# Kernel optimization log

Hardware: AMD Instinct MI355X
Metric: run time of the kernel (lower is better)

The kernel has to match this reference:

```python
import jax, jax.numpy as jnp
import numpy as np

N = 50000      # nodes
E = 800000     # edges
F_IN = 9       # node features
H = 128        # model_units
G = 64         # graphs in batch


def _lin_init(key, fan_in, fan_out):
    k1, k2 = jax.random.split(key)
    lim = 1.0 / np.sqrt(fan_in)
    W = jax.random.uniform(k1, (fan_in, fan_out), minval=-lim, maxval=lim, dtype=jnp.float32)
    b = jax.random.uniform(k2, (fan_out,), minval=-lim, maxval=lim, dtype=jnp.float32)
    return W, b


def setup_inputs() -> dict:
    key = jax.random.key(0)
    ks = jax.random.split(key, 12)
    x = jax.random.normal(ks[0], (N, F_IN), dtype=jnp.float32)
    edge_index = jax.random.randint(ks[1], (2, E), 0, N, dtype=jnp.int32)
    batch = jnp.sort(jax.random.randint(ks[2], (N,), 0, G, dtype=jnp.int32))
    W1, b1 = _lin_init(ks[3], F_IN, H)      # conv1 (GCN)
    W2, b2 = _lin_init(ks[4], H, H)         # conv2 (GCN, shared across layers)
    We1, be1 = _lin_init(ks[5], 2 * H, H)   # EdgeConv MLP layer 1
    We2, be2 = _lin_init(ks[6], H, H)       # EdgeConv MLP layer 2
    Wf1, bf1 = _lin_init(ks[7], H, H)
    Wf2, bf2 = _lin_init(ks[8], H, 32)
    Wf3, bf3 = _lin_init(ks[9], 32, 1)
    return {"x": x, "edge_index": edge_index, "batch": batch,
            "W1": W1, "b1": b1, "W2": W2, "b2": b2,
            "We1": We1, "be1": be1, "We2": We2, "be2": be2,
            "Wf1": Wf1, "bf1": bf1, "Wf2": Wf2, "bf2": bf2,
            "Wf3": Wf3, "bf3": bf3}


def _gcn(x, W, b, src, dst, dis):
    # GCNConv with implicit self-loops and symmetric normalization.
    h = x @ W                                              # [N,H]
    msg = h[src] * dis[src, None]                          # gather + scale
    agg = jax.ops.segment_sum(msg, dst, num_segments=N)    # scatter-add
    return dis[:, None] * agg + h * (dis * dis)[:, None] + b


def _edgeconv(x, We1, be1, We2, be2, src, dst):
    # EdgeConv: max_j MLP([x_i, x_j - x_i]) over incoming edges j->i.
    xi = x[dst]                                            # [E,H]
    xj = x[src]
    m = jnp.concatenate([xi, xj - xi], axis=-1)            # [E,2H]
    m = jax.nn.relu(m @ We1 + be1) @ We2 + be2             # [E,H]
    agg = jax.ops.segment_max(m, dst, num_segments=N)
    return jnp.where(jnp.isfinite(agg), agg, 0.0)          # isolated nodes -> 0


def reference(x, edge_index, batch, W1, b1, W2, b2, We1, be1, We2, be2,
              Wf1, bf1, Wf2, bf2, Wf3, bf3):
    src, dst = edge_index[0], edge_index[1]
    # degree (with self loop) for GCN normalization
    deg = jax.ops.segment_sum(jnp.ones((E,), jnp.float32), dst, num_segments=N) + 1.0
    dis = jax.lax.rsqrt(deg)

    h = jnp.tanh(_gcn(x, W1, b1, src, dst, dis))
    h = jnp.tanh(_edgeconv(h, We1, be1, We2, be2, src, dst))
    # model_layers = 3 -> loop body once, then final block (dropout = identity, eval)
    for _ in range(2):
        h = jnp.tanh(_gcn(h, W2, b2, src, dst, dis))
        h = jnp.tanh(_edgeconv(h, We1, be1, We2, be2, src, dst))

    h = jnp.tanh(h @ Wf1 + bf1)
    h = jnp.tanh(h @ Wf2 + bf2)
    h = h @ Wf3 + bf3                                      # [N,1]

    counts = jax.ops.segment_sum(jnp.ones((N,), jnp.float32), batch, num_segments=G)
    pooled = jax.ops.segment_sum(h, batch, num_segments=G) / jnp.maximum(counts, 1.0)[:, None]
    return jax.nn.sigmoid(pooled)                          # [G,1]
```

## Files before the change

kernel.cpp:

```cpp
#include <hip/hip_runtime.h>
#include <hip/hip_bf16.h>

#define N_NODES 50000
#define N_EDGES 800000
#define F_IN 9
#define H 128
#define G_GRAPHS 64
#define HH (H * H)
#define MAXT (N_EDGES / 16 + N_NODES)

typedef short bf16x8 __attribute__((ext_vector_type(8)));
typedef float f32x4 __attribute__((ext_vector_type(4)));

static __device__ inline short f2b(float f) {
    __hip_bfloat16 h = __float2bfloat16(f);
    return *reinterpret_cast<short*>(&h);
}
static __device__ inline float blo(unsigned u) { return __uint_as_float(u << 16); }
static __device__ inline float bhi(unsigned u) { return __uint_as_float(u & 0xFFFF0000u); }
static __device__ inline unsigned encodef(float f) {
    unsigned u = __float_as_uint(f);
    return (u & 0x80000000u) ? ~u : (u | 0x80000000u);
}
static __device__ inline float decodef(unsigned u) {
    return __uint_as_float((u & 0x80000000u) ? (u ^ 0x80000000u) : ~u);
}

__global__ __launch_bounds__(256) void k_detect(const unsigned* __restrict__ x, int* flag) {
    __shared__ int cnt;
    if (threadIdx.x == 0) cnt = 0;
    __syncthreads();
    unsigned u = x[threadIdx.x];
    int e = (u >> 7) & 0xFF;
    if (e >= 0x70 && e <= 0x83) atomicAdd(&cnt, 1);
    __syncthreads();
    if (threadIdx.x == 0) *flag = (cnt >= 128) ? 1 : 0;
}

struct CvtArgs { const void* src[15]; float* dst[15]; };

__global__ __launch_bounds__(256) void k_cvt_all(CvtArgs a, const int* __restrict__ flag) {
    const int sz[15] = {450000, 1152, 128, 16384, 128, 32768, 128, 16384, 128,
                        16384, 128, 4096, 32, 32, 1};
    int i = blockIdx.x * 256 + threadIdx.x;
    int fl = *flag;
    int base = 0;
    #pragma unroll
    for (int s = 0; s < 15; ++s) {
        if (i >= base && i < base + sz[s]) {
            int off = i - base;
            float v = fl ? __bfloat162float(((const __hip_bfloat16*)a.src[s])[off])
                         : ((const float*)a.src[s])[off];
            a.dst[s][off] = v;
        }
        base += sz[s];
    }
}

__global__ __launch_bounds__(256) void k_zero(float* p, int n) {
    int i = blockIdx.x * 256 + threadIdx.x;
    if (i < n) p[i] = 0.f;
}

__global__ __launch_bounds__(256) void k_sub(float* w) {
    int i = blockIdx.x * 256 + threadIdx.x;
    if (i < HH) w[i] -= w[HH + i];
}

__global__ __launch_bounds__(256) void k_prep(const float* __restrict__ W,
                                              short* __restrict__ Wf, int NT) {
    int tid = blockIdx.x * 256 + threadIdx.x;
    int total = 4 * NT * 64;
    if (tid >= total) return;
    int kc = tid / (NT * 64);
    int ct = (tid / 64) % NT;
    int lane = tid & 63;
    int Nc = NT * 16;
    int kb = kc * 32 + (lane >> 4) * 8;
    int col = ct * 16 + (lane & 15);
    #pragma unroll
    for (int j = 0; j < 8; ++j)
        Wf[tid * 8 + j] = f2b(W[(kb + j) * Nc + col]);
}

__global__ __launch_bounds__(256) void k_hist(const int* __restrict__ dst, int* cnt) {
    int e = blockIdx.x * 256 + threadIdx.x;
    if (e < N_EDGES) atomicAdd(&cnt[dst[e]], 1);
}

__global__ __launch_bounds__(256) void k_scan1(const int* __restrict__ deg, int* __restrict__ out,
                                               int* __restrict__ blockSums) {
    __shared__ int lds[256];
    int base = blockIdx.x * 2048;
    int t = threadIdx.x;
    int local[8];
    int s = 0;
    #pragma unroll
    for (int j = 0; j < 8; ++j) {
        int idx = base + t * 8 + j;
        int v = (idx < N_NODES) ? deg[idx] : 0;
        local[j] = s;
        s += v;
    }
    lds[t] = s;
    __syncthreads();
    if (t == 0) {
        int run = 0;
        for (int i = 0; i < 256; ++i) { int v = lds[i]; lds[i] = run; run += v; }
        blockSums[blockIdx.x] = run;
    }
    __syncthreads();
    int offs = lds[t];
    #pragma unroll
    for (int j = 0; j < 8; ++j) {
        int idx = base + t * 8 + j;
        if (idx < N_NODES) out[idx] = offs + local[j];
    }
}

__global__ void k_scan2(int* blockSums, int nb, int* rowptr) {
    int run = 0;
    for (int i = 0; i < nb; ++i) { int v = blockSums[i]; blockSums[i] = run; run += v; }
    rowptr[N_NODES] = N_EDGES;
}

__global__ void k_scan2t(int* blockSums, int nb, int* tstart, int* ntiles) {
    int run = 0;
    for (int i = 0; i < nb; ++i) { int v = blockSums[i]; blockSums[i] = run; run += v; }
    tstart[N_NODES] = run;
    *ntiles = run;
}

__global__ __launch_bounds__(256) void k_scan3(int* rowptr, const int* __restrict__ blockSums) {
    int idx = blockIdx.x * 256 + threadIdx.x;
    if (idx < N_NODES) rowptr[idx] += blockSums[idx >> 11];
}

__global__ __launch_bounds__(256) void k_scatter(const int* __restrict__ src, const int* __restrict__ dst,
                                                 const int* __restrict__ rowptr, int* cursor,
                                                 int* __restrict__ csr_src) {
    int e = blockIdx.x * 256 + threadIdx.x;
    if (e >= N_EDGES) return;
    int d = dst[e];
    int pos = rowptr[d] + atomicAdd(&cursor[d], 1);
    csr_src[pos] = src[e];
}

__global__ __launch_bounds__(256) void k_dis_tcnt(const int* __restrict__ rowptr, float* dis, int* tcnt) {
    int n = blockIdx.x * 256 + threadIdx.x;
    if (n < N_NODES) {
        int deg = rowptr[n + 1] - rowptr[n];
        dis[n] = rsqrtf((float)deg + 1.0f);
        tcnt[n] = (deg + 15) >> 4;
    }
}

__global__ __launch_bounds__(256) void k_tfill(const int* __restrict__ rowptr,
                                               const int* __restrict__ csr_src,
                                               const int* __restrict__ tstart,
                                               int* __restrict__ tileN,
                                               int* __restrict__ tileSrc) {
    int n = blockIdx.x * 256 + threadIdx.x;
    if (n >= N_NODES) return;
    int t0 = tstart[n], t1 = tstart[n + 1];
    int beg = rowptr[n], end = rowptr[n + 1];
    for (int t = t0; t < t1; ++t) {
        tileN[t] = n;
        int tb = beg + (t - t0) * 16;
        #pragma unroll 4
        for (int j = 0; j < 16; ++j) {
            int ei = tb + j;
            tileSrc[t * 16 + j] = csr_src[ei < end ? ei : end - 1];
        }
    }
}

__global__ __launch_bounds__(256) void k_counts(const int* __restrict__ batch, float* counts) {
    __shared__ float lc[G_GRAPHS];
    int tid = threadIdx.x;
    if (tid < G_GRAPHS) lc[tid] = 0.f;
    __syncthreads();
    int n = blockIdx.x * 256 + tid;
    if (n < N_NODES) atomicAdd(&lc[batch[n]], 1.0f);
    __syncthreads();
    if (tid < G_GRAPHS && lc[tid] > 0.f) atomicAdd(&counts[tid], lc[tid]);
}

__global__ __launch_bounds__(256) void k_gemm_f32bf_scale(const float* __restrict__ A,
                                                          const float* __restrict__ W,
                                                          const float* __restrict__ dis,
                                                          short* __restrict__ out, int M) {
    __shared__ float w_lds[F_IN * H];
    for (int i = threadIdx.x; i < F_IN * H; i += 256) w_lds[i] = W[i];
    __syncthreads();
    int row = blockIdx.x * 8 + threadIdx.x / 32;
    int c4 = (threadIdx.x & 31) << 2;
    if (row >= M) return;
    const float* a = A + (size_t)row * F_IN;
    float acc0 = 0.f, acc1 = 0.f, acc2 = 0.f, acc3 = 0.f;
    #pragma unroll
    for (int k = 0; k < F_IN; ++k) {
        float av = a[k];
        float4 w = *reinterpret_cast<const float4*>(&w_lds[k * H + c4]);
        acc0 = fmaf(av, w.x, acc0);
        acc1 = fmaf(av, w.y, acc1);
        acc2 = fmaf(av, w.z, acc2);
        acc3 = fmaf(av, w.w, acc3);
    }
    float dv = dis[row];
    short* op = &out[(size_t)row * H + c4];
    op[0] = f2b(acc0 * dv); op[1] = f2b(acc1 * dv);
    op[2] = f2b(acc2 * dv); op[3] = f2b(acc3 * dv);
}

__global__ __launch_bounds__(512) void k_gemm_dual(const short* __restrict__ A,
                                                   const short* __restrict__ WfU,
                                                   const short* __restrict__ WfV,
                                                   const float* __restrict__ be1,
                                                   short* __restrict__ U,
                                                   short* __restrict__ V, int M) {
    __shared__ short wl[32768];
    for (int i = threadIdx.x * 8; i < 16384; i += 4096) {
        *reinterpret_cast<f32x4*>(&wl[i])         = *reinterpret_cast<const f32x4*>(&WfU[i]);
        *reinterpret_cast<f32x4*>(&wl[16384 + i]) = *reinterpret_cast<const f32x4*>(&WfV[i]);
    }
    __syncthreads();
    int wv = threadIdx.x >> 6, lane = threadIdx.x & 63;
    int er = lane & 15, kg = lane >> 4;
    int row0 = (blockIdx.x * 8 + wv) * 16;
    if (row0 >= M) return;
    bf16x8 af[4];
    #pragma unroll
    for (int kc = 0; kc < 4; ++kc)
        af[kc] = *reinterpret_cast<const bf16x8*>(&A[(size_t)(row0 + er) * H + kc * 32 + kg * 8]);
    const f32x4 vzero = {0.f, 0.f, 0.f, 0.f};
    f32x4 acc[8];
    #pragma unroll
    for (int ct = 0; ct < 8; ++ct) acc[ct] = vzero;
    #pragma unroll
    for (int kc = 0; kc < 4; ++kc)
        #pragma unroll
        for (int ct = 0; ct < 8; ++ct) {
            bf16x8 bf = *reinterpret_cast<const bf16x8*>(&wl[((kc * 8 + ct) * 64 + lane) * 8]);
            acc[ct] = __builtin_amdgcn_mfma_f32_16x16x32_bf16(af[kc], bf, acc[ct], 0, 0, 0);
        }
    #pragma unroll
    for (int ct = 0; ct < 8; ++ct) {
        int col = ct * 16 + er;
        float bv = be1[col];
        #pragma unroll
        for (int r = 0; r < 4; ++r)
            U[(size_t)(row0 + kg * 4 + r) * H + col] = f2b(acc[ct][r] + bv);
    }
    #pragma unroll
    for (int ct = 0; ct < 8; ++ct) acc[ct] = vzero;
    #pragma unroll
    for (int kc = 0; kc < 4; ++kc)
        #pragma unroll
        for (int ct = 0; ct < 8; ++ct) {
            bf16x8 bf = *reinterpret_cast<const bf16x8*>(&wl[16384 + ((kc * 8 + ct) * 64 + lane) * 8]);
            acc[ct] = __builtin_amdgcn_mfma_f32_16x16x32_bf16(af[kc], bf, acc[ct], 0, 0, 0);
        }
    #pragma unroll
    for (int ct = 0; ct < 8; ++ct) {
        int col = ct * 16 + er;
        #pragma unroll
        for (int r = 0; r < 4; ++r)
            V[(size_t)(row0 + kg * 4 + r) * H + col] = f2b(acc[ct][r]);
    }
}

__global__ __launch_bounds__(512) void k_gemm_scale(const short* __restrict__ A,
                                                    const short* __restrict__ Wf,
                                                    const float* __restrict__ dis,
                                                    short* __restrict__ out, int M) {
    __shared__ short wl[16384];
    for (int i = threadIdx.x * 8; i < 16384; i += 4096)
        *reinterpret_cast<f32x4*>(&wl[i]) = *reinterpret_cast<const f32x4*>(&Wf[i]);
    __syncthreads();
    int wv = threadIdx.x >> 6, lane = threadIdx.x & 63;
    int er = lane & 15, kg = lane >> 4;
    int row0 = (blockIdx.x * 8 + wv) * 16;
    if (row0 >= M) return;
    bf16x8 af[4];
    #pragma unroll
    for (int kc = 0; kc < 4; ++kc)
        af[kc] = *reinterpret_cast<const bf16x8*>(&A[(size_t)(row0 + er) * H + kc * 32 + kg * 8]);
    const f32x4 vzero = {0.f, 0.f, 0.f, 0.f};
    f32x4 acc[8];
    #pragma unroll
    for (int ct = 0; ct < 8; ++ct) acc[ct] = vzero;
    #pragma unroll
    for (int kc = 0; kc < 4; ++kc)
        #pragma unroll
        for (int ct = 0; ct < 8; ++ct) {
            bf16x8 bf = *reinterpret_cast<const bf16x8*>(&wl[((kc * 8 + ct) * 64 + lane) * 8]);
            acc[ct] = __builtin_amdgcn_mfma_f32_16x16x32_bf16(af[kc], bf, acc[ct], 0, 0, 0);
        }
    float dv[4];
    #pragma unroll
    for (int r = 0; r < 4; ++r) dv[r] = dis[row0 + kg * 4 + r];
    #pragma unroll
    for (int ct = 0; ct < 8; ++ct) {
        int col = ct * 16 + er;
        #pragma unroll
        for (int r = 0; r < 4; ++r)
            out[(size_t)(row0 + kg * 4 + r) * H + col] = f2b(acc[ct][r] * dv[r]);
    }
}

__global__ __launch_bounds__(256) void k_gcn_fused(const int* __restrict__ rowptr,
                                                   const int* __restrict__ csr_src,
                                                   const short* __restrict__ hWs,
                                                   const float* __restrict__ dis,
                                                   const float* __restrict__ bias,
                                                   short* __restrict__ out) {
    int wv = threadIdx.x >> 6, lane = threadIdx.x & 63;
    const unsigned* hw = (const unsigned*)hWs;
    for (int n = blockIdx.x * 4 + wv; n < N_NODES; n += gridDim.x * 4) {
        int beg = rowptr[n], end = rowptr[n + 1];
        float a0 = 0.f, a1 = 0.f, b0 = 0.f, b1 = 0.f;
        float c0 = 0.f, c1 = 0.f, d0 = 0.f, d1 = 0.f;
        int e = beg;
        for (; e + 8 <= end; e += 8) {
            int s0 = csr_src[e],     s1 = csr_src[e + 1], s2 = csr_src[e + 2], s3 = csr_src[e + 3];
            int s4 = csr_src[e + 4], s5 = csr_src[e + 5], s6 = csr_src[e + 6], s7 = csr_src[e + 7];
            unsigned w0 = hw[(size_t)s0 * 64 + lane];
            unsigned w1 = hw[(size_t)s1 * 64 + lane];
            unsigned w2 = hw[(size_t)s2 * 64 + lane];
            unsigned w3 = hw[(size_t)s3 * 64 + lane];
            unsigned w4 = hw[(size_t)s4 * 64 + lane];
            unsigned w5 = hw[(size_t)s5 * 64 + lane];
            unsigned w6 = hw[(size_t)s6 * 64 + lane];
            unsigned w7 = hw[(size_t)s7 * 64 + lane];
            a0 += blo(w0); a1 += bhi(w0);
            b0 += blo(w1); b1 += bhi(w1);
            c0 += blo(w2); c1 += bhi(w2);
            d0 += blo(w3); d1 += bhi(w3);
            a0 += blo(w4); a1 += bhi(w4);
            b0 += blo(w5); b1 += bhi(w5);
            c0 += blo(w6); c1 += bhi(w6);
            d0 += blo(w7); d1 += bhi(w7);
        }
        for (; e + 4 <= end; e += 4) {
            int s0 = csr_src[e], s1 = csr_src[e + 1], s2 = csr_src[e + 2], s3 = csr_src[e + 3];
            unsigned w0 = hw[(size_t)s0 * 64 + lane];
            unsigned w1 = hw[(size_t)s1 * 64 + lane];
            unsigned w2 = hw[(size_t)s2 * 64 + lane];
            unsigned w3 = hw[(size_t)s3 * 64 + lane];
            a0 += blo(w0); a1 += bhi(w0);
            b0 += blo(w1); b1 += bhi(w1);
            c0 += blo(w2); c1 += bhi(w2);
            d0 += blo(w3); d1 += bhi(w3);
        }
        for (; e < end; ++e) {
            unsigned w = hw[(size_t)csr_src[e] * 64 + lane];
            a0 += blo(w); a1 += bhi(w);
        }
        float s0f = (a0 + b0) + (c0 + d0);
        float s1f = (a1 + b1) + (c1 + d1);
        float dn = dis[n];
        unsigned wn = hw[(size_t)n * 64 + lane];
        float r0 = tanhf(dn * (s0f + blo(wn)) + bias[lane * 2]);
        float r1 = tanhf(dn * (s1f + bhi(wn)) + bias[lane * 2 + 1]);
        unsigned o = (unsigned)(unsigned short)f2b(r0) | ((unsigned)(unsigned short)f2b(r1) << 16);
        *reinterpret_cast<unsigned*>(&out[(size_t)n * H + lane * 2]) = o;
    }
}

__global__ __launch_bounds__(512) void k_edge_tile(const int* __restrict__ tileN,
                                                   const int* __restrict__ tileSrc,
                                                   const int* __restrict__ ntilesp,
                                                   const short* __restrict__ U,
                                                   const short* __restrict__ V,
                                                   const short* __restrict__ We2f,
                                                   unsigned* aggEnc) {
    int nt = *ntilesp;
    if ((int)(blockIdx.x * 8) >= nt) return;
    __shared__ short wl[16384];
    for (int i = threadIdx.x * 8; i < 16384; i += 4096)
        *reinterpret_cast<f32x4*>(&wl[i]) = *reinterpret_cast<const f32x4*>(&We2f[i]);
    __syncthreads();
    int wv = threadIdx.x >> 6, lane = threadIdx.x & 63;
    int er = lane & 15, kg = lane >> 4, kseg = kg * 8;
    int tid = blockIdx.x * 8 + wv;
    if (tid >= nt) return;
    int n = tileN[tid];
    int s = tileSrc[tid * 16 + er];
    const f32x4 vzero = {0.f, 0.f, 0.f, 0.f};
    f32x4 acc[8];
    #pragma unroll
    for (int ct = 0; ct < 8; ++ct) acc[ct] = vzero;
    #pragma unroll
    for (int kc = 0; kc < 4; ++kc) {
        uint4 uu4 = *reinterpret_cast<const uint4*>(&U[(size_t)n * H + kc * 32 + kseg]);
        uint4 vv4 = *reinterpret_cast<const uint4*>(&V[(size_t)s * H + kc * 32 + kseg]);
        bf16x8 af;
        unsigned uu, vv;
        uu = uu4.x; vv = vv4.x;
        af[0] = f2b(fmaxf(blo(uu) + blo(vv), 0.f));
        af[1] = f2b(fmaxf(bhi(uu) + bhi(vv), 0.f));
        uu = uu4.y; vv = vv4.y;
        af[2] = f2b(fmaxf(blo(uu) + blo(vv), 0.f));
        af[3] = f2b(fmaxf(bhi(uu) + bhi(vv), 0.f));
        uu = uu4.z; vv = vv4.z;
        af[4] = f2b(fmaxf(blo(uu) + blo(vv), 0.f));
        af[5] = f2b(fmaxf(bhi(uu) + bhi(vv), 0.f));
        uu = uu4.w; vv = vv4.w;
        af[6] = f2b(fmaxf(blo(uu) + blo(vv), 0.f));
        af[7] = f2b(fmaxf(bhi(uu) + bhi(vv), 0.f));
        #pragma unroll
        for (int ct = 0; ct < 8; ++ct) {
            bf16x8 bf = *reinterpret_cast<const bf16x8*>(&wl[((kc * 8 + ct) * 64 + lane) * 8]);
            acc[ct] = __builtin_amdgcn_mfma_f32_16x16x32_bf16(af, bf, acc[ct], 0, 0, 0);
        }
    }
    float cm[8];
    #pragma unroll
    for (int ct = 0; ct < 8; ++ct) {
        float v = fmaxf(fmaxf(acc[ct][0], acc[ct][1]), fmaxf(acc[ct][2], acc[ct][3]));
        v = fmaxf(v, __shfl_xor(v, 16));
        v = fmaxf(v, __shfl_xor(v, 32));
        cm[ct] = v;
    }
    float vA, vB;
    if (kg == 0)      { vA = cm[0]; vB = cm[1]; }
    else if (kg == 1) { vA = cm[2]; vB = cm[3]; }
    else if (kg == 2) { vA = cm[4]; vB = cm[5]; }
    else              { vA = cm[6]; vB = cm[7]; }
    int colA = (kg * 2) * 16 + er;
    int colB = (kg * 2 + 1) * 16 + er;
    atomicMax(&aggEnc[(size_t)n * H + colA], encodef(vA));
    atomicMax(&aggEnc[(size_t)n * H + colB], encodef(vB));
}

__global__ __launch_bounds__(256) void k_edge_combine(const unsigned* __restrict__ aggEnc,
                                                      const float* __restrict__ be2,
                                                      short* __restrict__ out) {
    int i = blockIdx.x * 256 + threadIdx.x;
    if (i >= N_NODES * 64) return;
    int n = i >> 6, c2 = (i & 63) << 1;
    unsigned u0 = aggEnc[(size_t)n * H + c2];
    unsigned u1 = aggEnc[(size_t)n * H + c2 + 1];
    float r0 = tanhf(u0 ? (decodef(u0) + be2[c2]) : 0.f);
    float r1 = tanhf(u1 ? (decodef(u1) + be2[c2 + 1]) : 0.f);
    unsigned o = (unsigned)(unsigned short)f2b(r0) | ((unsigned)(unsigned short)f2b(r1) << 16);
    *reinterpret_cast<unsigned*>(&out[(size_t)n * H + c2]) = o;
}

__global__ __launch_bounds__(512) void k_final_mlp(const short* __restrict__ h,
                                                   const short* __restrict__ WfF1,
                                                   const short* __restrict__ WfF2,
                                                   const float* __restrict__ bf1,
                                                   const float* __restrict__ bf2,
                                                   const float* __restrict__ Wf3,
                                                   const float* __restrict__ bf3,
                                                   const int* __restrict__ batch,
                                                   float* pooled, int M) {
    __shared__ short wl1[16384];
    __shared__ short wl2[4096];
    __shared__ short tb[8][2048];
    __shared__ float lp[G_GRAPHS];
    for (int i = threadIdx.x * 8; i < 16384; i += 4096)
        *reinterpret_cast<f32x4*>(&wl1[i]) = *reinterpret_cast<const f32x4*>(&WfF1[i]);
    if (threadIdx.x < 512) {
        int i = threadIdx.x * 8;
        if (i < 4096)
            *reinterpret_cast<f32x4*>(&wl2[i]) = *reinterpret_cast<const f32x4*>(&WfF2[i]);
    }
    if (threadIdx.x < G_GRAPHS) lp[threadIdx.x] = 0.f;
    __syncthreads();
    int wv = threadIdx.x >> 6, lane = threadIdx.x & 63;
    int er = lane & 15, kg = lane >> 4;
    int row0 = (blockIdx.x * 8 + wv) * 16;
    bool active = row0 < M;
    const f32x4 vzero = {0.f, 0.f, 0.f, 0.f};
    if (active) {
        bf16x8 af[4];
        #pragma unroll
        for (int kc = 0; kc < 4; ++kc)
            af[kc] = *reinterpret_cast<const bf16x8*>(&h[(size_t)(row0 + er) * H + kc * 32 + kg * 8]);
        f32x4 acc[8];
        #pragma unroll
        for (int ct = 0; ct < 8; ++ct) acc[ct] = vzero;
        #pragma unroll
        for (int kc = 0; kc < 4; ++kc)
            #pragma unroll
            for (int ct = 0; ct < 8; ++ct) {
                bf16x8 bf = *reinterpret_cast<const bf16x8*>(&wl1[((kc * 8 + ct) * 64 + lane) * 8]);
                acc[ct] = __builtin_amdgcn_mfma_f32_16x16x32_bf16(af[kc], bf, acc[ct], 0, 0, 0);
            }
        #pragma unroll
        for (int ct = 0; ct < 8; ++ct) {
            int col = ct * 16 + er;
            float bv = bf1[col];
            #pragma unroll
            for (int r = 0; r < 4; ++r)
                tb[wv][(kg * 4 + r) * 128 + col] = f2b(tanhf(acc[ct][r] + bv));
        }
    }
    __syncthreads();
    if (active) {
        bf16x8 af2[4];
        #pragma unroll
        for (int kc = 0; kc < 4; ++kc)
            af2[kc] = *reinterpret_cast<const bf16x8*>(&tb[wv][er * 128 + kc * 32 + kg * 8]);
        f32x4 a2[2];
        a2[0] = vzero; a2[1] = vzero;
        #pragma unroll
        for (int kc = 0; kc < 4; ++kc)
            #pragma unroll
            for (int ct = 0; ct < 2; ++ct) {
                bf16x8 bf = *reinterpret_cast<const bf16x8*>(&wl2[((kc * 2 + ct) * 64 + lane) * 8]);
                a2[ct] = __builtin_amdgcn_mfma_f32_16x16x32_bf16(af2[kc], bf, a2[ct], 0, 0, 0);
            }
        float w3a = Wf3[er], w3b = Wf3[16 + er];
        float b2a = bf2[er], b2b = bf2[16 + er];
        float bf3v = bf3[0];
        float psum[4];
        #pragma unroll
        for (int r = 0; r < 4; ++r) {
            float f2a = tanhf(a2[0][r] + b2a);
            float f2c = tanhf(a2[1][r] + b2b);
            float p = f2a * w3a + f2c * w3b;
            p += __shfl_xor(p, 1);
            p += __shfl_xor(p, 2);
            p += __shfl_xor(p, 4);
            p += __shfl_xor(p, 8);
            psum[r] = p + bf3v;
        }
        if (er == 0) {
            #pragma unroll
            for (int r = 0; r < 4; ++r) {
                int n = row0 + kg * 4 + r;
                if (n < M) atomicAdd(&lp[batch[n]], psum[r]);
            }
        }
    }
    __syncthreads();
    if (threadIdx.x < G_GRAPHS && lp[threadIdx.x] != 0.f)
        atomicAdd(&pooled[threadIdx.x], lp[threadIdx.x]);
}

__global__ __launch_bounds__(64) void k_final(const float* pooled, const float* counts,
                                              void* out, const int* __restrict__ flag) {
    int g = threadIdx.x;
    if (g < G_GRAPHS) {
        float v = pooled[g] / fmaxf(counts[g], 1.0f);
        float s = 1.0f / (1.0f + expf(-v));
        if (*flag) ((__hip_bfloat16*)out)[g] = __float2bfloat16(s);
        else       ((float*)out)[g] = s;
    }
}

extern "C" void kernel_launch(void* const* d_in, const int* in_sizes, int n_in,
                              void* d_out, int out_size, void* d_ws, size_t ws_size,
                              hipStream_t stream) {
    const int* ei    = (const int*)d_in[1];
    const int* src   = ei;
    const int* dst   = ei + N_EDGES;
    const int* batch = (const int*)d_in[2];

    float* ws = (float*)d_ws;
    size_t off = 0;
    auto alloc = [&](size_t n) { off = (off + 3) & ~(size_t)3; float* p = ws + off; off += n; return p; };

    const size_t NH = (size_t)N_NODES * H;
    short* hb     = (short*)alloc(NH / 2);
    short* Ub     = (short*)alloc(NH / 2);
    short* Vb     = (short*)alloc(NH / 2);
    unsigned* aggEnc = (unsigned*)alloc(NH);
    float* xf     = alloc((size_t)N_NODES * F_IN);
    float* dis    = alloc(N_NODES);
    float* pooled = alloc(G_GRAPHS);
    float* counts = alloc(G_GRAPHS);
    int*   flag   = (int*)alloc(1);
    int*   rowptr = (int*)alloc(N_NODES + 1);
    int*   cursor = (int*)alloc(N_NODES);
    int*   csrsrc = (int*)alloc(N_EDGES);
    int*   bsums  = (int*)alloc(32);
    int*   bsums2 = (int*)alloc(32);
    int*   tstart = (int*)alloc(N_NODES + 1);
    int*   ntiles = (int*)alloc(1);
    int*   tileN  = (int*)alloc(MAXT);
    int*   tileSrc= (int*)alloc((size_t)MAXT * 16);

    float* W1  = alloc(F_IN * H);
    float* b1  = alloc(H);
    float* W2  = alloc(HH);
    float* b2  = alloc(H);
    float* We1 = alloc(2 * HH);
    float* be1 = alloc(H);
    float* We2 = alloc(HH);
    float* be2 = alloc(H);
    float* Wf1 = alloc(HH);
    float* bf1 = alloc(H);
    float* Wf2 = alloc(H * 32);
    float* bf2 = alloc(32);
    float* Wf3 = alloc(32);
    float* bf3 = alloc(4);
    short* WfU  = (short*)alloc(8192);
    short* WfV  = (short*)alloc(8192);
    short* WfW2 = (short*)alloc(8192);
    short* WfF1 = (short*)alloc(8192);
    short* WfF2 = (short*)alloc(2048);
    short* We2f = (short*)alloc(8192);

    const int eB    = (N_EDGES + 255) / 256;
    const int nB    = (N_NODES + 255) / 256;
    const int scanB = (N_NODES + 2047) / 2048;
    const int mfmaB = (N_NODES / 16 + 7) / 8;
    const int gcnB  = (N_NODES + 3) / 4;
    const int tileB = (MAXT + 7) / 8;
    const int zAggB = (int)((NH + 255) / 256);
    const int combB = (N_NODES * 64 + 255) / 256;

    k_detect<<<1, 256, 0, stream>>>((const unsigned*)d_in[0], flag);

    CvtArgs ca;
    const int srcIdx[15] = {0, 3, 4, 5, 6, 7, 8, 9, 10, 11, 12, 13, 14, 15, 16};
    float* dsts[15] = {xf, W1, b1, W2, b2, We1, be1, We2, be2, Wf1, bf1, Wf2, bf2, Wf3, bf3};
    for (int s = 0; s < 15; ++s) { ca.src[s] = d_in[srcIdx[s]]; ca.dst[s] = dsts[s]; }
    const int cvtTotal = 450000 + 1152 + 128 + 16384 + 128 + 32768 + 128 + 16384 + 128
                       + 16384 + 128 + 4096 + 32 + 32 + 1;
    k_cvt_all<<<(cvtTotal + 255) / 256, 256, 0, stream>>>(ca, flag);

    k_sub<<<(HH + 255) / 256, 256, 0, stream>>>(We1);
    k_prep<<<8, 256, 0, stream>>>(We1, WfU, 8);
    k_prep<<<8, 256, 0, stream>>>(We1 + HH, WfV, 8);
    k_prep<<<8, 256, 0, stream>>>(W2, WfW2, 8);
    k_prep<<<8, 256, 0, stream>>>(Wf1, WfF1, 8);
    k_prep<<<2, 256, 0, stream>>>(Wf2, WfF2, 2);
    k_prep<<<8, 256, 0, stream>>>(We2, We2f, 8);

    k_zero<<<nB, 256, 0, stream>>>((float*)cursor, N_NODES);
    k_hist<<<eB, 256, 0, stream>>>(dst, cursor);
    k_scan1<<<scanB, 256, 0, stream>>>(cursor, rowptr, bsums);
    k_scan2<<<1, 1, 0, stream>>>(bsums, scanB, rowptr);
    k_scan3<<<nB, 256, 0, stream>>>(rowptr, bsums);
    k_zero<<<nB, 256, 0, stream>>>((float*)cursor, N_NODES);
    k_scatter<<<eB, 256, 0, stream>>>(src, dst, rowptr, cursor, csrsrc);
    k_dis_tcnt<<<nB, 256, 0, stream>>>(rowptr, dis, cursor);
    k_zero<<<1, 256, 0, stream>>>(pooled, 2 * G_GRAPHS);
    k_counts<<<nB, 256, 0, stream>>>(batch, counts);

    k_scan1<<<scanB, 256, 0, stream>>>(cursor, tstart, bsums2);
    k_scan2t<<<1, 1, 0, stream>>>(bsums2, scanB, tstart, ntiles);
    k_scan3<<<nB, 256, 0, stream>>>(tstart, bsums2);
    k_tfill<<<nB, 256, 0, stream>>>(rowptr, csrsrc, tstart, tileN, tileSrc);

    k_gemm_f32bf_scale<<<(N_NODES + 7) / 8, 256, 0, stream>>>(xf, W1, dis, Ub, N_NODES);
    k_gcn_fused<<<gcnB, 256, 0, stream>>>(rowptr, csrsrc, Ub, dis, b1, hb);

    for (int iter = 0; iter < 3; ++iter) {
        k_gemm_dual<<<mfmaB, 512, 0, stream>>>(hb, WfU, WfV, be1, Ub, Vb, N_NODES);
        k_zero<<<zAggB, 256, 0, stream>>>((float*)aggEnc, (int)NH);
        k_edge_tile<<<tileB, 512, 0, stream>>>(tileN, tileSrc, ntiles, Ub, Vb, We2f, aggEnc);
        k_edge_combine<<<combB, 256, 0, stream>>>(aggEnc, be2, hb);
        if (iter < 2) {
            k_gemm_scale<<<mfmaB, 512, 0, stream>>>(hb, WfW2, dis, Ub, N_NODES);
            k_gcn_fused<<<gcnB, 256, 0, stream>>>(rowptr, csrsrc, Ub, dis, b2, hb);
        }
    }

    k_final_mlp<<<mfmaB, 512, 0, stream>>>(hb, WfF1, WfF2, bf1, bf2, Wf3, bf3,
                                           batch, pooled, N_NODES);
    k_final<<<1, 64, 0, stream>>>(pooled, counts, d_out, flag);
}
```

Baseline: 559.2 us.

## Fuse edge-combine into downstream GEMMs and merge setup kernels and scans

Removes the separate edge-combine kernel. The next GEMM (GCN scale, or the final MLP) now reads the max-encoded aggregate directly, decodes it, adds the bias, applies tanh and packs to bf16 in registers. This saves a full N×H write and re-read of the intermediate bf16 features each layer. It also merges the weight-prep kernels, the two prefix scans and the counts/zeroing into fewer launches, and uses the packed bf16 convert instruction. The trade-off is redundant decode and tanh work in each GEMM block, plus reading 4-byte aggregates instead of 2-byte features.

```diff
diff --git a/kernel.cpp b/kernel.cpp
--- a/kernel.cpp
+++ b/kernel.cpp
@@ -25,14 +25,21 @@
 static __device__ inline float decodef(unsigned u) {
     return __uint_as_float((u & 0x80000000u) ? (u ^ 0x80000000u) : ~u);
 }
-
-__global__ __launch_bounds__(256) void k_detect(const unsigned* __restrict__ x, int* flag) {
+static __device__ inline unsigned cvtpk(float lo, float hi) {
+    unsigned r;
+    asm("v_cvt_pk_bf16_f32 %0, %1, %2" : "=v"(r) : "v"(lo), "v"(hi));
+    return r;
+}
+
+__global__ __launch_bounds__(256) void k_detect(const unsigned* __restrict__ x, int* flag,
+                                                float* pooled, float* counts) {
     __shared__ int cnt;
     if (threadIdx.x == 0) cnt = 0;
     __syncthreads();
     unsigned u = x[threadIdx.x];
     int e = (u >> 7) & 0xFF;
     if (e >= 0x70 && e <= 0x83) atomicAdd(&cnt, 1);
+    if (threadIdx.x < G_GRAPHS) { pooled[threadIdx.x] = 0.f; counts[threadIdx.x] = 0.f; }
     __syncthreads();
     if (threadIdx.x == 0) *flag = (cnt >= 128) ? 1 : 0;
 }
@@ -62,14 +69,21 @@
     if (i < n) p[i] = 0.f;
 }
 
-__global__ __launch_bounds__(256) void k_sub(float* w) {
-    int i = blockIdx.x * 256 + threadIdx.x;
-    if (i < HH) w[i] -= w[HH + i];
-}
-
-__global__ __launch_bounds__(256) void k_prep(const float* __restrict__ W,
-                                              short* __restrict__ Wf, int NT) {
-    int tid = blockIdx.x * 256 + threadIdx.x;
+__global__ __launch_bounds__(256) void k_prep_all(const float* __restrict__ We1,
+                                                  const float* __restrict__ W2,
+                                                  const float* __restrict__ Wf1,
+                                                  const float* __restrict__ Wf2,
+                                                  const float* __restrict__ We2,
+                                                  short* WfU, short* WfV, short* WfW2,
+                                                  short* WfF1, short* WfF2, short* We2f) {
+    int b = blockIdx.x;
+    const float* W; const float* Wm = nullptr; short* out; int NT = 8; int tid;
+    if (b < 8)       { W = We1;      Wm = We1 + HH; out = WfU;  tid = b * 256 + threadIdx.x; }
+    else if (b < 16) { W = We1 + HH; out = WfV;  tid = (b - 8) * 256 + threadIdx.x; }
+    else if (b < 24) { W = W2;       out = WfW2; tid = (b - 16) * 256 + threadIdx.x; }
+    else if (b < 32) { W = Wf1;      out = WfF1; tid = (b - 24) * 256 + threadIdx.x; }
+    else if (b < 40) { W = We2;      out = We2f; tid = (b - 32) * 256 + threadIdx.x; }
+    else             { W = Wf2;      out = WfF2; NT = 2; tid = (b - 40) * 256 + threadIdx.x; }
     int total = 4 * NT * 64;
     if (tid >= total) return;
     int kc = tid / (NT * 64);
@@ -79,8 +93,11 @@
     int kb = kc * 32 + (lane >> 4) * 8;
     int col = ct * 16 + (lane & 15);
     #pragma unroll
-    for (int j = 0; j < 8; ++j)
-        Wf[tid * 8 + j] = f2b(W[(kb + j) * Nc + col]);
+    for (int j = 0; j < 8; ++j) {
+        float w = W[(kb + j) * Nc + col];
+        if (Wm) w -= Wm[(kb + j) * Nc + col];
+        out[tid * 8 + j] = f2b(w);
+    }
 }
 
 __global__ __launch_bounds__(256) void k_hist(const int* __restrict__ dst, int* cnt) {
@@ -88,52 +105,59 @@
     if (e < N_EDGES) atomicAdd(&cnt[dst[e]], 1);
 }
 
-__global__ __launch_bounds__(256) void k_scan1(const int* __restrict__ deg, int* __restrict__ out,
-                                               int* __restrict__ blockSums) {
-    __shared__ int lds[256];
+__global__ __launch_bounds__(256) void k_scan1d(const int* __restrict__ deg,
+                                                int* __restrict__ outA, int* __restrict__ outB,
+                                                int* __restrict__ bsA, int* __restrict__ bsB) {
+    __shared__ int ldsA[256], ldsB[256];
     int base = blockIdx.x * 2048;
     int t = threadIdx.x;
-    int local[8];
-    int s = 0;
+    int localA[8], localB[8];
+    int sA = 0, sB = 0;
     #pragma unroll
     for (int j = 0; j < 8; ++j) {
         int idx = base + t * 8 + j;
         int v = (idx < N_NODES) ? deg[idx] : 0;
-        local[j] = s;
-        s += v;
-    }
-    lds[t] = s;
+        int tc = (v + 15) >> 4;
+        localA[j] = sA; sA += v;
+        localB[j] = sB; sB += tc;
+    }
+    ldsA[t] = sA; ldsB[t] = sB;
     __syncthreads();
     if (t == 0) {
         int run = 0;
-        for (int i = 0; i < 256; ++i) { int v = lds[i]; lds[i] = run; run += v; }
-        blockSums[blockIdx.x] = run;
-    }
-    __syncthreads();
-    int offs = lds[t];
+        for (int i = 0; i < 256; ++i) { int v = ldsA[i]; ldsA[i] = run; run += v; }
+        bsA[blockIdx.x] = run;
+        run = 0;
+        for (int i = 0; i < 256; ++i) { int v = ldsB[i]; ldsB[i] = run; run += v; }
+        bsB[blockIdx.x] = run;
+    }
+    __syncthreads();
+    int oA = ldsA[t], oB = ldsB[t];
     #pragma unroll
     for (int j = 0; j < 8; ++j) {
         int idx = base + t * 8 + j;
-        if (idx < N_NODES) out[idx] = offs + local[j];
-    }
-}
-
-__global__ void k_scan2(int* blockSums, int nb, int* rowptr) {
+        if (idx < N_NODES) { outA[idx] = oA + localA[j]; outB[idx] = oB + localB[j]; }
+    }
+}
+
+__global__ void k_scan2d(int* bsA, int* bsB, int nb, int* rowptr, int* tstart, int* ntiles) {
     int run = 0;
-    for (int i = 0; i < nb; ++i) { int v = blockSums[i]; blockSums[i] = run; run += v; }
+    for (int i = 0; i < nb; ++i) { int v = bsA[i]; bsA[i] = run; run += v; }
     rowptr[N_NODES] = N_EDGES;
-}
-
-__global__ void k_scan2t(int* blockSums, int nb, int* tstart, int* ntiles) {
-    int run = 0;
-    for (int i = 0; i < nb; ++i) { int v = blockSums[i]; blockSums[i] = run; run += v; }
+    run = 0;
+    for (int i = 0; i < nb; ++i) { int v = bsB[i]; bsB[i] = run; run += v; }
     tstart[N_NODES] = run;
     *ntiles = run;
 }
 
-__global__ __launch_bounds__(256) void k_scan3(int* rowptr, const int* __restrict__ blockSums) {
+__global__ __launch_bounds__(256) void k_scan3d(int* rowptr, int* tstart,
+                                                const int* __restrict__ bsA,
+                                                const int* __restrict__ bsB) {
     int idx = blockIdx.x * 256 + threadIdx.x;
-    if (idx < N_NODES) rowptr[idx] += blockSums[idx >> 11];
+    if (idx < N_NODES) {
+        rowptr[idx] += bsA[idx >> 11];
+        tstart[idx] += bsB[idx >> 11];
+    }
 }
 
 __global__ __launch_bounds__(256) void k_scatter(const int* __restrict__ src, const int* __restrict__ dst,
@@ -146,13 +170,20 @@
     csr_src[pos] = src[e];
 }
 
-__global__ __launch_bounds__(256) void k_dis_tcnt(const int* __restrict__ rowptr, float* dis, int* tcnt) {
+__global__ __launch_bounds__(256) void k_dis_counts(const int* __restrict__ rowptr, float* dis,
+                                                    const int* __restrict__ batch, float* counts) {
+    __shared__ float lc[G_GRAPHS];
+    if (threadIdx.x < G_GRAPHS) lc[threadIdx.x] = 0.f;
+    __syncthreads();
     int n = blockIdx.x * 256 + threadIdx.x;
     if (n < N_NODES) {
         int deg = rowptr[n + 1] - rowptr[n];
         dis[n] = rsqrtf((float)deg + 1.0f);
-        tcnt[n] = (deg + 15) >> 4;
-    }
+        atomicAdd(&lc[batch[n]], 1.0f);
+    }
+    __syncthreads();
+    if (threadIdx.x < G_GRAPHS && lc[threadIdx.x] > 0.f)
+        atomicAdd(&counts[threadIdx.x], lc[threadIdx.x]);
 }
 
 __global__ __launch_bounds__(256) void k_tfill(const int* __restrict__ rowptr,
@@ -175,17 +206,6 @@
     }
 }
 
-__global__ __launch_bounds__(256) void k_counts(const int* __restrict__ batch, float* counts) {
-    __shared__ float lc[G_GRAPHS];
-    int tid = threadIdx.x;
-    if (tid < G_GRAPHS) lc[tid] = 0.f;
-    __syncthreads();
-    int n = blockIdx.x * 256 + tid;
-    if (n < N_NODES) atomicAdd(&lc[batch[n]], 1.0f);
-    __syncthreads();
-    if (tid < G_GRAPHS && lc[tid] > 0.f) atomicAdd(&counts[tid], lc[tid]);
-}
-
 __global__ __launch_bounds__(256) void k_gemm_f32bf_scale(const float* __restrict__ A,
                                                           const float* __restrict__ W,
                                                           const float* __restrict__ dis,
@@ -208,9 +228,8 @@
         acc3 = fmaf(av, w.w, acc3);
     }
     float dv = dis[row];
-    short* op = &out[(size_t)row * H + c4];
-    op[0] = f2b(acc0 * dv); op[1] = f2b(acc1 * dv);
-    op[2] = f2b(acc2 * dv); op[3] = f2b(acc3 * dv);
+    uint2 o = make_uint2(cvtpk(acc0 * dv, acc1 * dv), cvtpk(acc2 * dv, acc3 * dv));
+    *reinterpret_cast<uint2*>(&out[(size_t)row * H + c4]) = o;
 }
 
 __global__ __launch_bounds__(512) void k_gemm_dual(const short* __restrict__ A,
@@ -270,10 +289,11 @@
     }
 }
 
-__global__ __launch_bounds__(512) void k_gemm_scale(const short* __restrict__ A,
-                                                    const short* __restrict__ Wf,
-                                                    const float* __restrict__ dis,
-                                                    short* __restrict__ out, int M) {
+__global__ __launch_bounds__(512) void k_gemm_scale_agg(const unsigned* __restrict__ aggEnc,
+                                                        const float* __restrict__ be2,
+                                                        const short* __restrict__ Wf,
+                                                        const float* __restrict__ dis,
+                                                        short* __restrict__ out, int M) {
     __shared__ short wl[16384];
     for (int i = threadIdx.x * 8; i < 16384; i += 4096)
         *reinterpret_cast<f32x4*>(&wl[i]) = *reinterpret_cast<const f32x4*>(&Wf[i]);
@@ -284,8 +304,24 @@
     if (row0 >= M) return;
     bf16x8 af[4];
     #pragma unroll
-    for (int kc = 0; kc < 4; ++kc)
-        af[kc] = *reinterpret_cast<const bf16x8*>(&A[(size_t)(row0 + er) * H + kc * 32 + kg * 8]);
+    for (int kc = 0; kc < 4; ++kc) {
+        int basec = kc * 32 + kg * 8;
+        const unsigned* ap = &aggEnc[(size_t)(row0 + er) * H + basec];
+        uint4 q0 = *reinterpret_cast<const uint4*>(ap);
+        uint4 q1 = *reinterpret_cast<const uint4*>(ap + 4);
+        float f0 = q0.x ? tanhf(decodef(q0.x) + be2[basec + 0]) : 0.f;
+        float f1 = q0.y ? tanhf(decodef(q0.y) + be2[basec + 1]) : 0.f;
+        float f2 = q0.z ? tanhf(decodef(q0.z) + be2[basec + 2]) : 0.f;
+        float f3 = q0.w ? tanhf(decodef(q0.w) + be2[basec + 3]) : 0.f;
+        float f4 = q1.x ? tanhf(decodef(q1.x) + be2[basec + 4]) : 0.f;
+        float f5 = q1.y ? tanhf(decodef(q1.y) + be2[basec + 5]) : 0.f;
+        float f6 = q1.z ? tanhf(decodef(q1.z) + be2[basec + 6]) : 0.f;
+        float f7 = q1.w ? tanhf(decodef(q1.w) + be2[basec + 7]) : 0.f;
+        union { unsigned u[4]; bf16x8 v; } A;
+        A.u[0] = cvtpk(f0, f1); A.u[1] = cvtpk(f2, f3);
+        A.u[2] = cvtpk(f4, f5); A.u[3] = cvtpk(f6, f7);
+        af[kc] = A.v;
+    }
     const f32x4 vzero = {0.f, 0.f, 0.f, 0.f};
     f32x4 acc[8];
     #pragma unroll
@@ -363,8 +399,7 @@
         unsigned wn = hw[(size_t)n * 64 + lane];
         float r0 = tanhf(dn * (s0f + blo(wn)) + bias[lane * 2]);
         float r1 = tanhf(dn * (s1f + bhi(wn)) + bias[lane * 2 + 1]);
-        unsigned o = (unsigned)(unsigned short)f2b(r0) | ((unsigned)(unsigned short)f2b(r1) << 16);
-        *reinterpret_cast<unsigned*>(&out[(size_t)n * H + lane * 2]) = o;
+        *reinterpret_cast<unsigned*>(&out[(size_t)n * H + lane * 2]) = cvtpk(r0, r1);
     }
 }
 
@@ -395,24 +430,15 @@
     for (int kc = 0; kc < 4; ++kc) {
         uint4 uu4 = *reinterpret_cast<const uint4*>(&U[(size_t)n * H + kc * 32 + kseg]);
         uint4 vv4 = *reinterpret_cast<const uint4*>(&V[(size_t)s * H + kc * 32 + kseg]);
-        bf16x8 af;
-        unsigned uu, vv;
-        uu = uu4.x; vv = vv4.x;
-        af[0] = f2b(fmaxf(blo(uu) + blo(vv), 0.f));
-        af[1] = f2b(fmaxf(bhi(uu) + bhi(vv), 0.f));
-        uu = uu4.y; vv = vv4.y;
-        af[2] = f2b(fmaxf(blo(uu) + blo(vv), 0.f));
-        af[3] = f2b(fmaxf(bhi(uu) + bhi(vv), 0.f));
-        uu = uu4.z; vv = vv4.z;
-        af[4] = f2b(fmaxf(blo(uu) + blo(vv), 0.f));
-        af[5] = f2b(fmaxf(bhi(uu) + bhi(vv), 0.f));
-        uu = uu4.w; vv = vv4.w;
-        af[6] = f2b(fmaxf(blo(uu) + blo(vv), 0.f));
-        af[7] = f2b(fmaxf(bhi(uu) + bhi(vv), 0.f));
+        union { unsigned u[4]; bf16x8 v; } A;
+        A.u[0] = cvtpk(fmaxf(blo(uu4.x) + blo(vv4.x), 0.f), fmaxf(bhi(uu4.x) + bhi(vv4.x), 0.f));
+        A.u[1] = cvtpk(fmaxf(blo(uu4.y) + blo(vv4.y), 0.f), fmaxf(bhi(uu4.y) + bhi(vv4.y), 0.f));
+        A.u[2] = cvtpk(fmaxf(blo(uu4.z) + blo(vv4.z), 0.f), fmaxf(bhi(uu4.z) + bhi(vv4.z), 0.f));
+        A.u[3] = cvtpk(fmaxf(blo(uu4.w) + blo(vv4.w), 0.f), fmaxf(bhi(uu4.w) + bhi(vv4.w), 0.f));
         #pragma unroll
         for (int ct = 0; ct < 8; ++ct) {
             bf16x8 bf = *reinterpret_cast<const bf16x8*>(&wl[((kc * 8 + ct) * 64 + lane) * 8]);
-            acc[ct] = __builtin_amdgcn_mfma_f32_16x16x32_bf16(af, bf, acc[ct], 0, 0, 0);
+            acc[ct] = __builtin_amdgcn_mfma_f32_16x16x32_bf16(A.v, bf, acc[ct], 0, 0, 0);
         }
     }
     float cm[8];
@@ -434,36 +460,23 @@
     atomicMax(&aggEnc[(size_t)n * H + colB], encodef(vB));
 }
 
-__global__ __launch_bounds__(256) void k_edge_combine(const unsigned* __restrict__ aggEnc,
-                                                      const float* __restrict__ be2,
-                                                      short* __restrict__ out) {
-    int i = blockIdx.x * 256 + threadIdx.x;
-    if (i >= N_NODES * 64) return;
-    int n = i >> 6, c2 = (i & 63) << 1;
-    unsigned u0 = aggEnc[(size_t)n * H + c2];
-    unsigned u1 = aggEnc[(size_t)n * H + c2 + 1];
-    float r0 = tanhf(u0 ? (decodef(u0) + be2[c2]) : 0.f);
-    float r1 = tanhf(u1 ? (decodef(u1) + be2[c2 + 1]) : 0.f);
-    unsigned o = (unsigned)(unsigned short)f2b(r0) | ((unsigned)(unsigned short)f2b(r1) << 16);
-    *reinterpret_cast<unsigned*>(&out[(size_t)n * H + c2]) = o;
-}
-
-__global__ __launch_bounds__(512) void k_final_mlp(const short* __restrict__ h,
-                                                   const short* __restrict__ WfF1,
-                                                   const short* __restrict__ WfF2,
-                                                   const float* __restrict__ bf1,
-                                                   const float* __restrict__ bf2,
-                                                   const float* __restrict__ Wf3,
-                                                   const float* __restrict__ bf3,
-                                                   const int* __restrict__ batch,
-                                                   float* pooled, int M) {
+__global__ __launch_bounds__(512) void k_final_mlp_agg(const unsigned* __restrict__ aggEnc,
+                                                       const float* __restrict__ be2,
+                                                       const short* __restrict__ WfF1,
+                                                       const short* __restrict__ WfF2,
+                                                       const float* __restrict__ bf1,
+                                                       const float* __restrict__ bf2,
+                                                       const float* __restrict__ Wf3,
+                                                       const float* __restrict__ bf3,
+                                                       const int* __restrict__ batch,
+                                                       float* pooled, int M) {
     __shared__ short wl1[16384];
     __shared__ short wl2[4096];
     __shared__ short tb[8][2048];
     __shared__ float lp[G_GRAPHS];
     for (int i = threadIdx.x * 8; i < 16384; i += 4096)
         *reinterpret_cast<f32x4*>(&wl1[i]) = *reinterpret_cast<const f32x4*>(&WfF1[i]);
-    if (threadIdx.x < 512) {
+    {
         int i = threadIdx.x * 8;
         if (i < 4096)
             *reinterpret_cast<f32x4*>(&wl2[i]) = *reinterpret_cast<const f32x4*>(&WfF2[i]);
@@ -478,8 +491,24 @@
     if (active) {
         bf16x8 af[4];
         #pragma unroll
-        for (int kc = 0; kc < 4; ++kc)
-            af[kc] = *reinterpret_cast<const bf16x8*>(&h[(size_t)(row0 + er) * H + kc * 32 + kg * 8]);
+        for (int kc = 0; kc < 4; ++kc) {
+            int basec = kc * 32 + kg * 8;
+            const unsigned* ap = &aggEnc[(size_t)(row0 + er) * H + basec];
+            uint4 q0 = *reinterpret_cast<const uint4*>(ap);
+            uint4 q1 = *reinterpret_cast<const uint4*>(ap + 4);
+            float f0 = q0.x ? tanhf(decodef(q0.x) + be2[basec + 0]) : 0.f;
+            float f1 = q0.y ? tanhf(decodef(q0.y) + be2[basec + 1]) : 0.f;
+            float f2 = q0.z ? tanhf(decodef(q0.z) + be2[basec + 2]) : 0.f;
+            float f3 = q0.w ? tanhf(decodef(q0.w) + be2[basec + 3]) : 0.f;
+            float f4 = q1.x ? tanhf(decodef(q1.x) + be2[basec + 4]) : 0.f;
+            float f5 = q1.y ? tanhf(decodef(q1.y) + be2[basec + 5]) : 0.f;
+            float f6 = q1.z ? tanhf(decodef(q1.z) + be2[basec + 6]) : 0.f;
+            float f7 = q1.w ? tanhf(decodef(q1.w) + be2[basec + 7]) : 0.f;
+            union { unsigned u[4]; bf16x8 v; } A;
+            A.u[0] = cvtpk(f0, f1); A.u[1] = cvtpk(f2, f3);
+            A.u[2] = cvtpk(f4, f5); A.u[3] = cvtpk(f6, f7);
+            af[kc] = A.v;
+        }
         f32x4 acc[8];
         #pragma unroll
         for (int ct = 0; ct < 8; ++ct) acc[ct] = vzero;
@@ -613,9 +642,8 @@
     const int gcnB  = (N_NODES + 3) / 4;
     const int tileB = (MAXT + 7) / 8;
     const int zAggB = (int)((NH + 255) / 256);
-    const int combB = (N_NODES * 64 + 255) / 256;
-
-    k_detect<<<1, 256, 0, stream>>>((const unsigned*)d_in[0], flag);
+
+    k_detect<<<1, 256, 0, stream>>>((const unsigned*)d_in[0], flag, pooled, counts);
 
     CvtArgs ca;
     const int srcIdx[15] = {0, 3, 4, 5, 6, 7, 8, 9, 10, 11, 12, 13, 14, 15, 16};
@@ -625,28 +653,17 @@
                        + 16384 + 128 + 4096 + 32 + 32 + 1;
     k_cvt_all<<<(cvtTotal + 255) / 256, 256, 0, stream>>>(ca, flag);
 
-    k_sub<<<(HH + 255) / 256, 256, 0, stream>>>(We1);
-    k_prep<<<8, 256, 0, stream>>>(We1, WfU, 8);
-    k_prep<<<8, 256, 0, stream>>>(We1 + HH, WfV, 8);
-    k_prep<<<8, 256, 0, stream>>>(W2, WfW2, 8);
-    k_prep<<<8, 256, 0, stream>>>(Wf1, WfF1, 8);
-    k_prep<<<2, 256, 0, stream>>>(Wf2, WfF2, 2);
-    k_prep<<<8, 256, 0, stream>>>(We2, We2f, 8);
+    k_prep_all<<<42, 256, 0, stream>>>(We1, W2, Wf1, Wf2, We2,
+                                       WfU, WfV, WfW2, WfF1, WfF2, We2f);
 
     k_zero<<<nB, 256, 0, stream>>>((float*)cursor, N_NODES);
     k_hist<<<eB, 256, 0, stream>>>(dst, cursor);
-    k_scan1<<<scanB, 256, 0, stream>>>(cursor, rowptr, bsums);
-    k_scan2<<<1, 1, 0, stream>>>(bsums, scanB, rowptr);
-    k_scan3<<<nB, 256, 0, stream>>>(rowptr, bsums);
+    k_scan1d<<<scanB, 256, 0, stream>>>(cursor, rowptr, tstart, bsums, bsums2);
+    k_scan2d<<<1, 1, 0, stream>>>(bsums, bsums2, scanB, rowptr, tstart, ntiles);
+    k_scan3d<<<nB, 256, 0, stream>>>(rowptr, tstart, bsums, bsums2);
     k_zero<<<nB, 256, 0, stream>>>((float*)cursor, N_NODES);
     k_scatter<<<eB, 256, 0, stream>>>(src, dst, rowptr, cursor, csrsrc);
-    k_dis_tcnt<<<nB, 256, 0, stream>>>(rowptr, dis, cursor);
-    k_zero<<<1, 256, 0, stream>>>(pooled, 2 * G_GRAPHS);
-    k_counts<<<nB, 256, 0, stream>>>(batch, counts);
-
-    k_scan1<<<scanB, 256, 0, stream>>>(cursor, tstart, bsums2);
-    k_scan2t<<<1, 1, 0, stream>>>(bsums2, scanB, tstart, ntiles);
-    k_scan3<<<nB, 256, 0, stream>>>(tstart, bsums2);
+    k_dis_counts<<<nB, 256, 0, stream>>>(rowptr, dis, batch, counts);
     k_tfill<<<nB, 256, 0, stream>>>(rowptr, csrsrc, tstart, tileN, tileSrc);
 
     k_gemm_f32bf_scale<<<(N_NODES + 7) / 8, 256, 0, stream>>>(xf, W1, dis, Ub, N_NODES);
@@ -656,14 +673,13 @@
         k_gemm_dual<<<mfmaB, 512, 0, stream>>>(hb, WfU, WfV, be1, Ub, Vb, N_NODES);
         k_zero<<<zAggB, 256, 0, stream>>>((float*)aggEnc, (int)NH);
         k_edge_tile<<<tileB, 512, 0, stream>>>(tileN, tileSrc, ntiles, Ub, Vb, We2f, aggEnc);
-        k_edge_combine<<<combB, 256, 0, stream>>>(aggEnc, be2, hb);
         if (iter < 2) {
-            k_gemm_scale<<<mfmaB, 512, 0, stream>>>(hb, WfW2, dis, Ub, N_NODES);
+            k_gemm_scale_agg<<<mfmaB, 512, 0, stream>>>(aggEnc, be2, WfW2, dis, Ub, N_NODES);
             k_gcn_fused<<<gcnB, 256, 0, stream>>>(rowptr, csrsrc, Ub, dis, b2, hb);
         }
     }
 
-    k_final_mlp<<<mfmaB, 512, 0, stream>>>(hb, WfF1, WfF2, bf1, bf2, Wf3, bf3,
-                                           batch, pooled, N_NODES);
+    k_final_mlp_agg<<<mfmaB, 512, 0, stream>>>(aggEnc, be2, WfF1, WfF2, bf1, bf2, Wf3, bf3,
+                                               batch, pooled, N_NODES);
     k_final<<<1, 64, 0, stream>>>(pooled, counts, d_out, flag);
 }
```

Result: faster. 529.0 us (-5.4%).
